# Performance work log

Measured on AMD Instinct MI355X. Metric: run time of the kernel, lower is better.

The kernel has to match this reference:

```python
import jax, jax.numpy as jnp
import numpy as np

DIM = 1024
DIM_FEAT = 384
HIDDEN = 1024
HEADS = 16
D_HEAD = HIDDEN // HEADS
SCALE = D_HEAD ** -0.5
EPS = 1e-5


def _layernorm(x, g, b):
    mu = jnp.mean(x, axis=-1, keepdims=True)
    var = jnp.var(x, axis=-1, keepdims=True)
    return (x - mu) * jax.lax.rsqrt(var + EPS) * g + b


def _split_heads(t):
    b, n, _ = t.shape
    return t.reshape(b, n, HEADS, D_HEAD).transpose(0, 2, 1, 3)  # b h n d


def _merge_heads(t):
    b, h, n, d = t.shape
    return t.transpose(0, 2, 1, 3).reshape(b, n, h * d)


def _attn(q, k, v):
    dots = jnp.einsum('bhnd,bhmd->bhnm', q, k) * SCALE
    attn = jax.nn.softmax(dots, axis=-1)
    return jnp.einsum('bhnm,bhmd->bhnd', attn, v)


def setup_inputs() -> dict:
    key = jax.random.key(0)
    ks = jax.random.split(key, 10)
    B, N = 2, 2048
    s = lambda fan: 1.0 / np.sqrt(fan)
    return {
        'x': jax.random.normal(ks[0], (B, N, DIM), jnp.float32),
        'feature': jax.random.normal(ks[1], (B, N, DIM_FEAT), jnp.float32),
        'norm_g': jnp.ones((DIM,), jnp.float32),
        'norm_b': jnp.zeros((DIM,), jnp.float32),
        'W_cq': jax.random.normal(ks[2], (DIM, HIDDEN), jnp.float32) * s(DIM),
        'W_ckv': jax.random.normal(ks[3], (DIM_FEAT, 2 * HIDDEN), jnp.float32) * s(DIM_FEAT),
        'W_sqkv': jax.random.normal(ks[4], (DIM, 3 * HIDDEN), jnp.float32) * s(DIM),
        'ffn_g': jnp.ones((DIM,), jnp.float32),
        'ffn_b': jnp.zeros((DIM,), jnp.float32),
        'W1': jax.random.normal(ks[5], (DIM, 4 * DIM), jnp.float32) * s(DIM),
        'b1': jnp.zeros((4 * DIM,), jnp.float32),
        'W2': jax.random.normal(ks[6], (4 * DIM, DIM), jnp.float32) * s(4 * DIM),
        'b2': jnp.zeros((DIM,), jnp.float32),
    }


def reference(x, feature, norm_g, norm_b, W_cq, W_ckv, W_sqkv, ffn_g, ffn_b, W1, b1, W2, b2):
    # cross attention
    xn = _layernorm(x, norm_g, norm_b)
    q = _split_heads(xn @ W_cq)
    kv = feature @ W_ckv
    k, v = jnp.split(kv, 2, axis=-1)
    cross = _merge_heads(_attn(q, _split_heads(k), _split_heads(v))) + x
    # self attention (shared norm)
    cn = _layernorm(cross, norm_g, norm_b)
    qkv = cn @ W_sqkv
    sq, sk, sv = (_split_heads(t) for t in jnp.split(qkv, 3, axis=-1))
    self_tok = _merge_heads(_attn(sq, sk, sv)) + cross
    # FFN with its own layernorm
    h = _layernorm(self_tok, ffn_g, ffn_b)
    h = jax.nn.gelu(h @ W1 + b1, approximate=False)
    out = h @ W2 + b2
    return out + self_tok
```

## Files before the change

### kernel.cpp

```cpp
#include <hip/hip_runtime.h>
#include <math.h>
#include <stdint.h>

typedef __attribute__((ext_vector_type(8)))  short   short8;
typedef __attribute__((ext_vector_type(4)))  short   short4v;
typedef __attribute__((ext_vector_type(8)))  __bf16  bf16x8;
typedef __attribute__((ext_vector_type(4)))  float   f32x4;
typedef __attribute__((ext_vector_type(16))) float   f32x16;

__device__ __forceinline__ unsigned short f2b(float f) {
    union { float f; unsigned u; } v; v.f = f;
    unsigned r = v.u + 0x7FFF + ((v.u >> 16) & 1);
    return (unsigned short)(r >> 16);
}

__device__ __forceinline__ f32x4 mfma_bf16(bf16x8 a, bf16x8 b, f32x4 c) {
    return __builtin_amdgcn_mfma_f32_16x16x32_bf16(a, b, c, 0, 0, 0);
}

__device__ __forceinline__ f32x16 mfma32(bf16x8 a, bf16x8 b, f32x16 c) {
    return __builtin_amdgcn_mfma_f32_32x32x16_bf16(a, b, c, 0, 0, 0);
}

__device__ __forceinline__ unsigned cvt_pk_bf16(float lo, float hi) {
    unsigned r;
    asm volatile("v_cvt_pk_bf16_f32 %0, %1, %2" : "=v"(r) : "v"(lo), "v"(hi));
    return r;
}

__device__ __forceinline__ void gload_lds16(const unsigned short* g, unsigned short* l) {
    __builtin_amdgcn_global_load_lds(
        (const __attribute__((address_space(1))) void*)g,
        (__attribute__((address_space(3))) void*)l,
        16, 0, 0);
}

template <int N>
__device__ __forceinline__ void wait_vmcnt() {
    if constexpr (N == 0)       asm volatile("s_waitcnt vmcnt(0)" ::: "memory");
    else if constexpr (N == 6)  asm volatile("s_waitcnt vmcnt(6)" ::: "memory");
    else if constexpr (N == 8)  asm volatile("s_waitcnt vmcnt(8)" ::: "memory");
    else                        static_assert(N == 0 || N == 6 || N == 8, "add vmcnt case");
}

#define QSCALE 0.18033688011112042592f

__global__ __launch_bounds__(256) void wconv_t(const float* __restrict__ W,
                                               unsigned short* __restrict__ Wt,
                                               int K, int N) {
    __shared__ float tile[32][33];
    int bk = blockIdx.x * 32;
    int bn = blockIdx.y * 32;
    int tx = threadIdx.x & 31, ty = threadIdx.x >> 5;
#pragma unroll
    for (int i = 0; i < 4; ++i) {
        int r = ty + i * 8;
        tile[r][tx] = W[(size_t)(bk + r) * N + bn + tx];
    }
    __syncthreads();
#pragma unroll
    for (int i = 0; i < 4; ++i) {
        int r = ty + i * 8;
        Wt[(size_t)(bn + r) * K + bk + tx] = f2b(tile[tx][r]);
    }
}

__global__ __launch_bounds__(256) void fconv(const float* __restrict__ in,
                                             unsigned short* __restrict__ out, int n4) {
    int i = blockIdx.x * 256 + threadIdx.x;
    if (i >= n4) return;
    f32x4 v = ((const f32x4*)in)[i];
    short4v o;
    o.x = (short)f2b(v.x); o.y = (short)f2b(v.y);
    o.z = (short)f2b(v.z); o.w = (short)f2b(v.w);
    ((short4v*)out)[i] = o;
}

__global__ __launch_bounds__(256) void lnorm(const float* __restrict__ x,
                                             const float* __restrict__ g,
                                             const float* __restrict__ bta,
                                             unsigned short* __restrict__ out) {
    int row = blockIdx.x;
    const f32x4* xr = (const f32x4*)(x + (size_t)row * 1024);
    int t = threadIdx.x;
    f32x4 v = xr[t];
    float s  = v.x + v.y + v.z + v.w;
    float s2 = v.x * v.x + v.y * v.y + v.z * v.z + v.w * v.w;
#pragma unroll
    for (int m = 1; m < 64; m <<= 1) {
        s  += __shfl_xor(s, m);
        s2 += __shfl_xor(s2, m);
    }
    __shared__ float rs[8];
    int w = t >> 6;
    if ((t & 63) == 0) { rs[w] = s; rs[4 + w] = s2; }
    __syncthreads();
    s  = rs[0] + rs[1] + rs[2] + rs[3];
    s2 = rs[4] + rs[5] + rs[6] + rs[7];
    float mean = s * (1.0f / 1024.0f);
    float var  = s2 * (1.0f / 1024.0f) - mean * mean;
    float rstd = rsqrtf(var + 1e-5f);
    f32x4 gv = ((const f32x4*)g)[t];
    f32x4 bv = ((const f32x4*)bta)[t];
    short4v o;
    o.x = (short)f2b((v.x - mean) * rstd * gv.x + bv.x);
    o.y = (short)f2b((v.y - mean) * rstd * gv.y + bv.y);
    o.z = (short)f2b((v.z - mean) * rstd * gv.z + bv.z);
    o.w = (short)f2b((v.w - mean) * rstd * gv.w + bv.w);
    ((short4v*)(out + (size_t)row * 1024))[t] = o;
}

template <int WM, int WN, int MI, int NI, int EPI, bool SCQ>
__global__ __launch_bounds__(WM * WN * 64, 2)
void gemm8(const unsigned short* __restrict__ A,
           const unsigned short* __restrict__ Bt,
           void* __restrict__ C,
           const float* __restrict__ bias,
           const float* __restrict__ resid,
           int M, int N, int K, int scale_cols) {
    constexpr int BM = WM * MI * 16;
    constexpr int BN = WN * NI * 16;
    constexpr int THREADS = WM * WN * 64;
    constexpr int ROWS = THREADS / 8;
    constexpr int IA = BM / ROWS;
    constexpr int IB = BN / ROWS;

    const int nwg = gridDim.x;
    const int nby = N / BN;
    int flat = blockIdx.x;
    int wk = (flat & 7) * (nwg >> 3) + (flat >> 3);
    const int m0 = (wk / nby) * BM;
    const int n0 = (wk % nby) * BN;

    __shared__ unsigned short As[2][BM * 64];
    __shared__ unsigned short Bs[2][BN * 64];

    const int tid  = threadIdx.x;
    const int lane = tid & 63;
    const int wid  = tid >> 6;
    const int wm = wid / WN, wn = wid % WN;
    const int l15 = lane & 15, q4 = lane >> 4, xw = lane & 7;

    const int sr = tid >> 3;
    const int sg = (tid & 7) ^ (sr & 7);

    const unsigned short* ag = A  + (size_t)(m0 + sr) * K + sg * 8;
    const unsigned short* bg = Bt + (size_t)(n0 + sr) * K + sg * 8;

    f32x4 acc[MI][NI] = {};

    auto STAGE = [&](int d, int t) {
        const int k0 = t * 64;
#pragma unroll
        for (int i = 0; i < IA; ++i)
            gload_lds16(ag + (size_t)(i * ROWS) * K + k0, &As[d][i * ROWS * 64 + tid * 8]);
#pragma unroll
        for (int i = 0; i < IB; ++i)
            gload_lds16(bg + (size_t)(i * ROWS) * K + k0, &Bs[d][i * ROWS * 64 + tid * 8]);
    };

    const int NT = K >> 6;
    STAGE(0, 0);

    for (int t = 0; t < NT; ++t) {
        const int c = t & 1;
        if (t + 1 < NT) STAGE(c ^ 1, t + 1);
        __builtin_amdgcn_sched_barrier(0);
        if (t + 1 < NT) wait_vmcnt<IA + IB>();
        else            wait_vmcnt<0>();
        __builtin_amdgcn_s_barrier();
        __builtin_amdgcn_sched_barrier(0);
#pragma unroll
        for (int h = 0; h < 2; ++h) {
            bf16x8 a[MI], b[NI];
            const int gsl = h * 4 + q4;
#pragma unroll
            for (int mi = 0; mi < MI; ++mi)
                a[mi] = *(const bf16x8*)&As[c][(wm * MI * 16 + mi * 16 + l15) * 64 + ((gsl ^ xw) << 3)];
#pragma unroll
            for (int ni = 0; ni < NI; ++ni)
                b[ni] = *(const bf16x8*)&Bs[c][(wn * NI * 16 + ni * 16 + l15) * 64 + ((gsl ^ xw) << 3)];
            __builtin_amdgcn_s_setprio(1);
#pragma unroll
            for (int mi = 0; mi < MI; ++mi)
#pragma unroll
                for (int ni = 0; ni < NI; ++ni)
                    acc[mi][ni] = mfma_bf16(a[mi], b[ni], acc[mi][ni]);
            __builtin_amdgcn_s_setprio(0);
        }
        __builtin_amdgcn_sched_barrier(0);
        __builtin_amdgcn_s_barrier();
    }

    const int rb = m0 + wm * MI * 16 + q4 * 4;
    const int cb = n0 + wn * NI * 16 + l15;
    float bv[NI];
    if (EPI >= 1) {
#pragma unroll
        for (int ni = 0; ni < NI; ++ni) bv[ni] = bias[cb + ni * 16];
    }
#pragma unroll
    for (int mi = 0; mi < MI; ++mi) {
#pragma unroll
        for (int r = 0; r < 4; ++r) {
            const int row = rb + mi * 16 + r;
#pragma unroll
            for (int ni = 0; ni < NI; ++ni) {
                const int col = cb + ni * 16;
                float v = acc[mi][ni][r];
                if (EPI == 0) {
                    if (SCQ && col < scale_cols) v *= QSCALE;
                    ((unsigned short*)C)[(size_t)row * N + col] = f2b(v);
                } else if (EPI == 1) {
                    v += bv[ni];
                    v = 0.5f * v * (1.0f + erff(v * 0.70710678118f));
                    ((unsigned short*)C)[(size_t)row * N + col] = f2b(v);
                } else {
                    v += bv[ni] + resid[(size_t)row * N + col];
                    ((float*)C)[(size_t)row * N + col] = v;
                }
            }
        }
    }
}

__global__ __launch_bounds__(256) void vtrans(const unsigned short* __restrict__ src,
                                              unsigned short* __restrict__ dst,
                                              int src_stride, int col_off) {
    int n0 = blockIdx.x * 64;
    int bh = blockIdx.y;
    int b = bh >> 4, h = bh & 15;
    __shared__ unsigned short t[64][65];
    int tx = threadIdx.x & 63, ty = threadIdx.x >> 6;
    const unsigned short* s = src + (size_t)(b * 2048 + n0) * src_stride + col_off + h * 64;
#pragma unroll
    for (int i = 0; i < 16; ++i) {
        int n = ty * 16 + i;
        t[n][tx] = s[(size_t)n * src_stride + tx];
    }
    __syncthreads();
    unsigned short* d = dst + (size_t)bh * 64 * 2048 + n0;
#pragma unroll
    for (int i = 0; i < 16; ++i) {
        int dd = ty * 16 + i;
        d[(size_t)dd * 2048 + tx] = t[tx][dd];
    }
}

__global__ __launch_bounds__(128) void attn(const unsigned short* __restrict__ Q, int q_stride, int q_off,
                                            const unsigned short* __restrict__ Kp, int k_stride, int k_off,
                                            const unsigned short* __restrict__ Vt,
                                            const float* __restrict__ res,
                                            float* __restrict__ out) {
    const int bid = blockIdx.x;
    const int slot = bid >> 3;
    const int bh = (bid & 7) * 4 + (slot >> 5);
    const int qt = slot & 31;
    const int b = bh >> 4, h = bh & 15;
    const int lane = threadIdx.x & 63, w = threadIdx.x >> 6;
    const int l31 = lane & 31, l5 = lane >> 5;

    __shared__ unsigned short lds[2][8192];

    const int q0 = qt * 64 + w * 32;

    const unsigned short* qp = Q + (size_t)(b * 2048 + q0 + l31) * q_stride + q_off + h * 64 + l5 * 8;
    bf16x8 qf[4];
#pragma unroll
    for (int i = 0; i < 4; ++i) qf[i] = *(const bf16x8*)&qp[i * 16];

    const unsigned short* kg = Kp + (size_t)(b * 2048) * k_stride + k_off + h * 64;
    const unsigned short* vg = Vt + (size_t)bh * 64 * 2048;

    f32x16 oacc[2] = {};
    float m = -1e30f, l = 0.f;

    auto STAGE = [&](int d, int t) {
        const int n0 = t * 64;
#pragma unroll
        for (int j = 0; j < 4; ++j) {
            const int g = w * 4 + j;
            gload_lds16(kg + (size_t)(n0 + lane) * k_stride + g * 8, &lds[d][g * 512]);
            gload_lds16(vg + (size_t)lane * 2048 + n0 + g * 8,       &lds[d][4096 + g * 512]);
        }
    };

    STAGE(0, 0);
    asm volatile("s_waitcnt vmcnt(0)" ::: "memory");
    __builtin_amdgcn_s_barrier();

    for (int t = 0; t < 32; ++t) {
        const int cur = t & 1;
        if (t + 1 < 32) STAGE(cur ^ 1, t + 1);
        __builtin_amdgcn_sched_barrier(0);
        if (t + 1 < 32) wait_vmcnt<8>();
        else            wait_vmcnt<0>();
        __builtin_amdgcn_s_barrier();
        __builtin_amdgcn_sched_barrier(0);

        const unsigned short* Kc = &lds[cur][0];
        const unsigned short* Vc = &lds[cur][4096];

        bf16x8 kf[2][4];
#pragma unroll
        for (int ks = 0; ks < 2; ++ks)
#pragma unroll
            for (int i = 0; i < 4; ++i)
                kf[ks][i] = *(const bf16x8*)&Kc[(i * 2 + l5) * 512 + ks * 256 + l31 * 8];

        f32x16 s0 = {}, s1 = {};
        __builtin_amdgcn_s_setprio(1);
#pragma unroll
        for (int i = 0; i < 4; ++i) s0 = mfma32(kf[0][i], qf[i], s0);
#pragma unroll
        for (int i = 0; i < 4; ++i) s1 = mfma32(kf[1][i], qf[i], s1);
        __builtin_amdgcn_s_setprio(0);

        bf16x8 vf[2][4];
#pragma unroll
        for (int dh = 0; dh < 2; ++dh)
#pragma unroll
            for (int c = 0; c < 4; ++c)
                vf[dh][c] = *(const bf16x8*)&Vc[(c * 2 + l5) * 512 + dh * 256 + l31 * 8];

        float tr[16];
#pragma unroll
        for (int r = 0; r < 16; ++r) tr[r] = fmaxf(s0[r], s1[r]);
#pragma unroll
        for (int off = 8; off >= 1; off >>= 1)
#pragma unroll
            for (int r = 0; r < off; ++r) tr[r] = fmaxf(tr[r], tr[r + off]);
        float mx = fmaxf(tr[0], __shfl_xor(tr[0], 32));
        if (!__all(mx - m <= 8.f)) {
            float mnew = fmaxf(m, mx);
            float al = __builtin_amdgcn_exp2f(m - mnew);
            m = mnew;
            l *= al;
#pragma unroll
            for (int dh = 0; dh < 2; ++dh)
#pragma unroll
                for (int r = 0; r < 16; ++r) oacc[dh][r] *= al;
        }
        float p0[16], p1[16];
#pragma unroll
        for (int r = 0; r < 16; ++r) p0[r] = __builtin_amdgcn_exp2f(s0[r] - m);
#pragma unroll
        for (int r = 0; r < 16; ++r) p1[r] = __builtin_amdgcn_exp2f(s1[r] - m);
        float sm[16];
#pragma unroll
        for (int r = 0; r < 16; ++r) sm[r] = p0[r] + p1[r];
#pragma unroll
        for (int off = 8; off >= 1; off >>= 1)
#pragma unroll
            for (int r = 0; r < off; ++r) sm[r] += sm[r + off];
        l += sm[0] + __shfl_xor(sm[0], 32);

        bf16x8 pf[4];
#pragma unroll
        for (int half = 0; half < 2; ++half) {
            const float* p = half ? p1 : p0;
#pragma unroll
            for (int c = 0; c < 2; ++c) {
                unsigned a0 = cvt_pk_bf16(p[8 * c + 0], p[8 * c + 1]);
                unsigned a1 = cvt_pk_bf16(p[8 * c + 4], p[8 * c + 5]);
                unsigned b0 = cvt_pk_bf16(p[8 * c + 2], p[8 * c + 3]);
                unsigned b1 = cvt_pk_bf16(p[8 * c + 6], p[8 * c + 7]);
                asm volatile("v_permlane32_swap_b32 %0, %1" : "+v"(a0), "+v"(a1));
                asm volatile("v_permlane32_swap_b32 %0, %1" : "+v"(b0), "+v"(b1));
                union { unsigned u[4]; bf16x8 v; } pu;
                pu.u[0] = a0; pu.u[1] = b0; pu.u[2] = a1; pu.u[3] = b1;
                pf[half * 2 + c] = pu.v;
            }
        }

        __builtin_amdgcn_s_setprio(1);
#pragma unroll
        for (int dh = 0; dh < 2; ++dh)
#pragma unroll
            for (int c = 0; c < 4; ++c)
                oacc[dh] = mfma32(vf[dh][c], pf[c], oacc[dh]);
        __builtin_amdgcn_s_setprio(0);

        __builtin_amdgcn_s_barrier();
    }

    const float inv = 1.0f / l;
    const size_t rowoff = (size_t)(b * 2048 + q0 + l31) * 1024 + h * 64;
#pragma unroll
    for (int dh = 0; dh < 2; ++dh) {
#pragma unroll
        for (int g = 0; g < 4; ++g) {
            const int col = dh * 32 + g * 8 + l5 * 4;
            f32x4 rv = *(const f32x4*)&res[rowoff + col];
            f32x4 ov;
#pragma unroll
            for (int r = 0; r < 4; ++r) ov[r] = oacc[dh][g * 4 + r] * inv + rv[r];
            *(f32x4*)&out[rowoff + col] = ov;
        }
    }
}

extern "C" void kernel_launch(void* const* d_in, const int* in_sizes, int n_in,
                              void* d_out, int out_size, void* d_ws, size_t ws_size,
                              hipStream_t stream) {
    const float* x      = (const float*)d_in[0];
    const float* feat   = (const float*)d_in[1];
    const float* norm_g = (const float*)d_in[2];
    const float* norm_b = (const float*)d_in[3];
    const float* W_cq   = (const float*)d_in[4];
    const float* W_ckv  = (const float*)d_in[5];
    const float* W_sqkv = (const float*)d_in[6];
    const float* ffn_g  = (const float*)d_in[7];
    const float* ffn_b  = (const float*)d_in[8];
    const float* W1     = (const float*)d_in[9];
    const float* b1     = (const float*)d_in[10];
    const float* W2     = (const float*)d_in[11];
    const float* b2     = (const float*)d_in[12];
    float* out = (float*)d_out;

    char* ws = (char*)d_ws;
    unsigned short* wq_t   = (unsigned short*)(ws + (size_t)(0u)   * (1u << 20));
    unsigned short* wkv_t  = (unsigned short*)(ws + (size_t)(2u)   * (1u << 20));
    unsigned short* wqkv_t = (unsigned short*)(ws + (size_t)(4u)   * (1u << 20));
    unsigned short* w1_t   = (unsigned short*)(ws + (size_t)(10u)  * (1u << 20));
    unsigned short* w2_t   = (unsigned short*)(ws + (size_t)(18u)  * (1u << 20));
    unsigned short* featb  = (unsigned short*)(ws + (size_t)(26u)  * (1u << 20));
    unsigned short* t0     = (unsigned short*)(ws + (size_t)(29u)  * (1u << 20));
    float*          cross  = (float*)        (ws + (size_t)(37u)  * (1u << 20));
    unsigned short* qb     = (unsigned short*)(ws + (size_t)(53u)  * (1u << 20));
    unsigned short* kvb    = (unsigned short*)(ws + (size_t)(61u)  * (1u << 20));
    unsigned short* qkvb   = (unsigned short*)(ws + (size_t)(77u)  * (1u << 20));
    unsigned short* vtb    = (unsigned short*)(ws + (size_t)(101u) * (1u << 20));
    unsigned short* h1     = (unsigned short*)(ws + (size_t)(53u)  * (1u << 20));

    wconv_t<<<dim3(1024 / 32, 1024 / 32), 256, 0, stream>>>(W_cq,   wq_t,   1024, 1024);
    wconv_t<<<dim3(384 / 32,  2048 / 32), 256, 0, stream>>>(W_ckv,  wkv_t,  384,  2048);
    wconv_t<<<dim3(1024 / 32, 3072 / 32), 256, 0, stream>>>(W_sqkv, wqkv_t, 1024, 3072);
    wconv_t<<<dim3(1024 / 32, 4096 / 32), 256, 0, stream>>>(W1,     w1_t,   1024, 4096);
    wconv_t<<<dim3(4096 / 32, 1024 / 32), 256, 0, stream>>>(W2,     w2_t,   4096, 1024);
    fconv<<<dim3((4096 * 384 / 4) / 256), 256, 0, stream>>>(feat, featb, 4096 * 384 / 4);

    lnorm<<<4096, 256, 0, stream>>>(x, norm_g, norm_b, t0);
    gemm8<2, 2, 4, 2, 0, true ><<<512, 256, 0, stream>>>(t0,    wq_t,  qb,  nullptr, nullptr, 4096, 1024, 1024, 1024);
    gemm8<2, 2, 4, 4, 0, false><<<512, 256, 0, stream>>>(featb, wkv_t, kvb, nullptr, nullptr, 4096, 2048, 384,  0);
    vtrans<<<dim3(32, 32), 256, 0, stream>>>(kvb, vtb, 2048, 1024);
    attn<<<1024, 128, 0, stream>>>(qb, 1024, 0, kvb, 2048, 0, vtb, x, cross);

    lnorm<<<4096, 256, 0, stream>>>(cross, norm_g, norm_b, t0);
    gemm8<2, 2, 4, 2, 0, true ><<<1536, 256, 0, stream>>>(t0, wqkv_t, qkvb, nullptr, nullptr, 4096, 3072, 1024, 1024);
    vtrans<<<dim3(32, 32), 256, 0, stream>>>(qkvb, vtb, 3072, 2048);
    attn<<<1024, 128, 0, stream>>>(qkvb, 3072, 0, qkvb, 3072, 1024, vtb, cross, out);

    lnorm<<<4096, 256, 0, stream>>>(out, ffn_g, ffn_b, t0);
    gemm8<2, 2, 4, 4, 1, false><<<1024, 256, 0, stream>>>(t0, w1_t, h1, b1, nullptr, 4096, 4096, 1024, 0);
    gemm8<2, 2, 4, 2, 2, false><<<512, 256, 0, stream>>>(h1, w2_t, out, b2, (const float*)out, 4096, 1024, 4096, 0);
}
```

Measured before the change: 384.8 us.

## Widen attention blocks to 4 waves with triple-buffered, XOR-swizzled K/V staging

The attention kernel now runs 256-thread blocks covering 128 query rows, so each staged K/V tile is shared by four waves instead of two and the launch drops to 512 blocks. K/V staging moves from double to triple buffering with prefetch two tiles ahead, and the wait counts are adjusted accordingly. The LDS layout changes to row-major 64x64 tiles with an XOR swizzle to avoid bank conflicts on fragment reads. In exchange, LDS use rises to 48 KB per block and there are fewer blocks, which may reduce occupancy and tail balance.

```diff
diff --git a/kernel.cpp b/kernel.cpp
--- a/kernel.cpp
+++ b/kernel.cpp
@@ -38,9 +38,10 @@
 template <int N>
 __device__ __forceinline__ void wait_vmcnt() {
     if constexpr (N == 0)       asm volatile("s_waitcnt vmcnt(0)" ::: "memory");
+    else if constexpr (N == 4)  asm volatile("s_waitcnt vmcnt(4)" ::: "memory");
     else if constexpr (N == 6)  asm volatile("s_waitcnt vmcnt(6)" ::: "memory");
     else if constexpr (N == 8)  asm volatile("s_waitcnt vmcnt(8)" ::: "memory");
-    else                        static_assert(N == 0 || N == 6 || N == 8, "add vmcnt case");
+    else                        static_assert(N == 0 || N == 4 || N == 6 || N == 8, "add vmcnt case");
 }
 
 #define QSCALE 0.18033688011112042592f
@@ -247,22 +248,23 @@
     }
 }
 
-__global__ __launch_bounds__(128) void attn(const unsigned short* __restrict__ Q, int q_stride, int q_off,
+__global__ __launch_bounds__(256) void attn(const unsigned short* __restrict__ Q, int q_stride, int q_off,
                                             const unsigned short* __restrict__ Kp, int k_stride, int k_off,
                                             const unsigned short* __restrict__ Vt,
                                             const float* __restrict__ res,
                                             float* __restrict__ out) {
     const int bid = blockIdx.x;
     const int slot = bid >> 3;
-    const int bh = (bid & 7) * 4 + (slot >> 5);
-    const int qt = slot & 31;
+    const int bh = (bid & 7) * 4 + (slot >> 4);
+    const int qt = slot & 15;
     const int b = bh >> 4, h = bh & 15;
     const int lane = threadIdx.x & 63, w = threadIdx.x >> 6;
     const int l31 = lane & 31, l5 = lane >> 5;
 
-    __shared__ unsigned short lds[2][8192];
-
-    const int q0 = qt * 64 + w * 32;
+    __shared__ unsigned short Ks[3][64 * 64];
+    __shared__ unsigned short Vs[3][64 * 64];
+
+    const int q0 = qt * 128 + w * 32;
 
     const unsigned short* qp = Q + (size_t)(b * 2048 + q0 + l31) * q_stride + q_off + h * 64 + l5 * 8;
     bf16x8 qf[4];
@@ -272,41 +274,46 @@
     const unsigned short* kg = Kp + (size_t)(b * 2048) * k_stride + k_off + h * 64;
     const unsigned short* vg = Vt + (size_t)bh * 64 * 2048;
 
+    const int sgrow = lane >> 3;
+    const int sgcol = (((lane & 7) ^ sgrow) << 3);
+
     f32x16 oacc[2] = {};
     float m = -1e30f, l = 0.f;
 
+    const int kxor = (l31 & 7) << 3;
+
     auto STAGE = [&](int d, int t) {
-        const int n0 = t * 64;
-#pragma unroll
-        for (int j = 0; j < 4; ++j) {
-            const int g = w * 4 + j;
-            gload_lds16(kg + (size_t)(n0 + lane) * k_stride + g * 8, &lds[d][g * 512]);
-            gload_lds16(vg + (size_t)lane * 2048 + n0 + g * 8,       &lds[d][4096 + g * 512]);
+        const int n0s = t * 64;
+#pragma unroll
+        for (int t8 = 0; t8 < 2; ++t8) {
+            const int rb = w * 16 + t8 * 8;
+            gload_lds16(kg + (size_t)(n0s + rb + sgrow) * k_stride + sgcol, &Ks[d][rb * 64]);
+            gload_lds16(vg + (size_t)(rb + sgrow) * 2048 + n0s + sgcol,     &Vs[d][rb * 64]);
         }
     };
 
     STAGE(0, 0);
-    asm volatile("s_waitcnt vmcnt(0)" ::: "memory");
-    __builtin_amdgcn_s_barrier();
+    STAGE(1, 1);
 
     for (int t = 0; t < 32; ++t) {
-        const int cur = t & 1;
-        if (t + 1 < 32) STAGE(cur ^ 1, t + 1);
+        const int cur = t % 3;
+        if (t + 2 < 32) STAGE((t + 2) % 3, t + 2);
         __builtin_amdgcn_sched_barrier(0);
-        if (t + 1 < 32) wait_vmcnt<8>();
-        else            wait_vmcnt<0>();
+        if (t + 2 < 32)      wait_vmcnt<8>();
+        else if (t + 1 < 32) wait_vmcnt<4>();
+        else                 wait_vmcnt<0>();
         __builtin_amdgcn_s_barrier();
         __builtin_amdgcn_sched_barrier(0);
 
-        const unsigned short* Kc = &lds[cur][0];
-        const unsigned short* Vc = &lds[cur][4096];
+        const unsigned short* Kc = &Ks[cur][0];
+        const unsigned short* Vc = &Vs[cur][0];
 
         bf16x8 kf[2][4];
 #pragma unroll
         for (int ks = 0; ks < 2; ++ks)
 #pragma unroll
             for (int i = 0; i < 4; ++i)
-                kf[ks][i] = *(const bf16x8*)&Kc[(i * 2 + l5) * 512 + ks * 256 + l31 * 8];
+                kf[ks][i] = *(const bf16x8*)&Kc[(ks * 32 + l31) * 64 + ((i * 16 + l5 * 8) ^ kxor)];
 
         f32x16 s0 = {}, s1 = {};
         __builtin_amdgcn_s_setprio(1);
@@ -321,7 +328,7 @@
         for (int dh = 0; dh < 2; ++dh)
 #pragma unroll
             for (int c = 0; c < 4; ++c)
-                vf[dh][c] = *(const bf16x8*)&Vc[(c * 2 + l5) * 512 + dh * 256 + l31 * 8];
+                vf[dh][c] = *(const bf16x8*)&Vc[(dh * 32 + l31) * 64 + ((c * 16 + l5 * 8) ^ kxor)];
 
         float tr[16];
 #pragma unroll
@@ -444,12 +451,12 @@
     gemm8<2, 2, 4, 2, 0, true ><<<512, 256, 0, stream>>>(t0,    wq_t,  qb,  nullptr, nullptr, 4096, 1024, 1024, 1024);
     gemm8<2, 2, 4, 4, 0, false><<<512, 256, 0, stream>>>(featb, wkv_t, kvb, nullptr, nullptr, 4096, 2048, 384,  0);
     vtrans<<<dim3(32, 32), 256, 0, stream>>>(kvb, vtb, 2048, 1024);
-    attn<<<1024, 128, 0, stream>>>(qb, 1024, 0, kvb, 2048, 0, vtb, x, cross);
+    attn<<<512, 256, 0, stream>>>(qb, 1024, 0, kvb, 2048, 0, vtb, x, cross);
 
     lnorm<<<4096, 256, 0, stream>>>(cross, norm_g, norm_b, t0);
     gemm8<2, 2, 4, 2, 0, true ><<<1536, 256, 0, stream>>>(t0, wqkv_t, qkvb, nullptr, nullptr, 4096, 3072, 1024, 1024);
     vtrans<<<dim3(32, 32), 256, 0, stream>>>(qkvb, vtb, 3072, 2048);
-    attn<<<1024, 128, 0, stream>>>(qkvb, 3072, 0, qkvb, 3072, 1024, vtb, cross, out);
+    attn<<<512, 256, 0, stream>>>(qkvb, 3072, 0, qkvb, 3072, 1024, vtb, cross, out);
 
     lnorm<<<4096, 256, 0, stream>>>(out, ffn_g, ffn_b, t0);
     gemm8<2, 2, 4, 4, 1, false><<<1024, 256, 0, stream>>>(t0, w1_t, h1, b1, nullptr, 4096, 4096, 1024, 0);
```

Result: faster. 354.0 us (-8.0%).
